# Optimization experiments

Hardware: AMD Instinct MI355X
Metric: run time of the kernel (lower is better)

## Reference

```python
import jax, jax.numpy as jnp
import numpy as np

EPS = 1e-5

def layer_norm(x, w):
    mu = x.mean(-1, keepdims=True)
    var = x.var(-1, keepdims=True)
    return (x - mu) * jax.lax.rsqrt(var + EPS) * w

def multihead_norm(x, w):
    # x: (B,S,NH,DH) -> group norm per head, elementwise weight over NH*DH features
    mu = x.mean(-1, keepdims=True)
    var = x.var(-1, keepdims=True)
    xn = (x - mu) * jax.lax.rsqrt(var + EPS)
    B, S, NH, DH = x.shape
    return xn.reshape(B, S, NH * DH) * w

def causal_conv1d(x, W, b):
    # x: (B,S,C), W: (C,K) depthwise causal conv, bias b: (C,)
    C, K = W.shape
    ker = W.T[:, None, :]  # (K,1,C) in WIO layout
    y = jax.lax.conv_general_dilated(x, ker, (1,), [(K - 1, 0)],
                                     dimension_numbers=('NWC', 'WIO', 'NWC'),
                                     feature_group_count=C)
    return y + b

def headwise_linear(x, W):
    # block-diagonal linear; W: (nblocks, out, in)
    nb, o, i = W.shape
    B, S, F = x.shape
    y = jnp.einsum('bsni,noi->bsno', x.reshape(B, S, nb, i), W)
    return y.reshape(B, S, nb * o)

def mlstm_block(x, ln_w, up_W, conv_W, conv_b, q_W, k_W, v_W, ig_W, ig_b, fg_W, fg_b, on_w, skip, down_W):
    B, S, E = x.shape
    I = up_W.shape[1] // 2
    NH = ig_W.shape[0]
    DH = I // NH
    xn = layer_norm(x, ln_w)
    up = xn @ up_W                       # (B,S,2I)
    xm, z = up[..., :I], up[..., I:]
    xc = jax.nn.silu(causal_conv1d(xm, conv_W, conv_b))
    q = headwise_linear(xc, q_W)
    k = headwise_linear(xc, k_W)
    v = headwise_linear(xm, v_W)        # values come from the pre-conv branch
    gin = jnp.concatenate([q, k, v], -1)  # (B,S,3I)
    ig = (gin @ ig_W.T + ig_b).transpose(0, 2, 1)  # (B,NH,S)
    fg = (gin @ fg_W.T + fg_b).transpose(0, 2, 1)
    qh = q.reshape(B, S, NH, DH).transpose(0, 2, 1, 3)
    kh = k.reshape(B, S, NH, DH).transpose(0, 2, 1, 3)
    vh = v.reshape(B, S, NH, DH).transpose(0, 2, 1, 3)
    # parallel stabilized mLSTM (matrix memory)
    logf = jax.nn.log_sigmoid(fg)
    cs = jnp.concatenate([jnp.zeros_like(logf[..., :1]), jnp.cumsum(logf, -1)], -1)  # (B,NH,S+1)
    lf = cs[..., 1:, None] - cs[..., None, 1:]   # (B,NH,S,S): sum of log f over (t, s]
    mask = jnp.tril(jnp.ones((S, S), bool))
    log_D = jnp.where(mask, lf + ig[:, :, None, :], -jnp.inf)
    max_log_D = log_D.max(-1, keepdims=True)
    D = jnp.exp(log_D - max_log_D)
    qk = jnp.einsum('bhsd,bhtd->bhst', qh, kh) * (DH ** -0.5)
    C = qk * D
    normalizer = jnp.maximum(jnp.abs(C.sum(-1, keepdims=True)), jnp.exp(-max_log_D))
    h = jnp.einsum('bhst,bhtd->bhsd', C / (normalizer + 1e-6), vh)
    h = multihead_norm(h.transpose(0, 2, 1, 3), on_w)  # (B,S,I)
    h = (h + skip * xc) * jax.nn.silu(z)
    return x + h @ down_W

def slstm_block(x, ln_w, conv_W, conv_b, gates_W, R, bias, gn_w, ffn_ln_w, ffn_up_W, ffn_down_W):
    B, S, E = x.shape
    NH, DH = R.shape[0], R.shape[1]
    xn = layer_norm(x, ln_w)
    xc = jax.nn.silu(causal_conv1d(xn, conv_W, conv_b))
    xh = xn.reshape(B, S, NH, DH)
    xch = xc.reshape(B, S, NH, DH)
    i_pre = jnp.einsum('bsnd,nod->bsno', xch, gates_W[0])  # i,f gates see conv branch
    f_pre = jnp.einsum('bsnd,nod->bsno', xch, gates_W[1])
    z_pre = jnp.einsum('bsnd,nod->bsno', xh, gates_W[2])
    o_pre = jnp.einsum('bsnd,nod->bsno', xh, gates_W[3])
    gx = jnp.stack([i_pre, f_pre, z_pre, o_pre], 3) + bias  # (B,S,NH,4,DH)
    def step(carry, g):
        h, c, n, m = carry
        raw = g + jnp.einsum('bnd,ndg->bng', h, R).reshape(B, NH, 4, DH)
        ir, fr, zr, og = raw[:, :, 0], raw[:, :, 1], raw[:, :, 2], raw[:, :, 3]
        logfplusm = m + jax.nn.log_sigmoid(fr)
        m_new = jnp.maximum(ir, logfplusm)
        i = jnp.exp(ir - m_new)
        f = jnp.exp(logfplusm - m_new)
        c_new = f * c + i * jnp.tanh(zr)
        n_new = f * n + i
        h_new = jax.nn.sigmoid(og) * c_new / n_new
        return (h_new, c_new, n_new, m_new), h_new
    z0 = jnp.zeros((B, NH, DH), x.dtype)
    _, hs = jax.lax.scan(step, (z0, z0, z0, z0), gx.transpose(1, 0, 2, 3, 4))
    y = multihead_norm(hs.transpose(1, 0, 2, 3), gn_w)  # (B,S,E)
    x = x + y
    xn2 = layer_norm(x, ffn_ln_w)
    gpre, upp = jnp.split(xn2 @ ffn_up_W, 2, -1)
    return x + (jax.nn.gelu(gpre, approximate=False) * upp) @ ffn_down_W

def forward(x, m_ln_w, m_up_W, m_conv_W, m_conv_b, m_q_W, m_k_W, m_v_W, m_ig_W, m_ig_b, m_fg_W, m_fg_b, m_outnorm_w, m_skip, m_down_W, s_ln_w, s_conv_W, s_conv_b, s_gates_W, s_R, s_bias, s_gn_w, s_ffn_ln_w, s_ffn_up_W, s_ffn_down_W, post_norm_w, fc_W, fc_b):
    mi = 0
    for blk in range(7):  # slstm_at=[1]
        if blk == 1:
            x = slstm_block(x, s_ln_w, s_conv_W, s_conv_b, s_gates_W, s_R, s_bias, s_gn_w, s_ffn_ln_w, s_ffn_up_W, s_ffn_down_W)
        else:
            x = mlstm_block(x, m_ln_w[mi], m_up_W[mi], m_conv_W[mi], m_conv_b[mi], m_q_W[mi], m_k_W[mi], m_v_W[mi], m_ig_W[mi], m_ig_b[mi], m_fg_W[mi], m_fg_b[mi], m_outnorm_w[mi], m_skip[mi], m_down_W[mi])
            mi += 1
    x = layer_norm(x, post_norm_w)
    return x[:, -1, :] @ fc_W + fc_b

def setup_inputs():
    key = jax.random.key(0)
    ks = jax.random.split(key, 18)
    B, S, E = 16, 512, 128
    I, NH = 256, 4
    DHs = E // NH
    FF = 192
    NB = 6
    r = lambda k, shape, sc: jax.random.normal(k, shape, jnp.float32) * sc
    return dict(
        x=r(ks[0], (B, S, E), 1.0),
        m_ln_w=jnp.ones((NB, E), jnp.float32),
        m_up_W=r(ks[1], (NB, E, 2 * I), E ** -0.5),
        m_conv_W=r(ks[2], (NB, I, 4), 0.3),
        m_conv_b=jnp.zeros((NB, I), jnp.float32),
        m_q_W=r(ks[3], (NB, 64, 4, 4), 0.5),
        m_k_W=r(ks[4], (NB, 64, 4, 4), 0.5),
        m_v_W=r(ks[5], (NB, 64, 4, 4), 0.5),
        m_ig_W=r(ks[6], (NB, NH, 3 * I), 0.1 * (3 * I) ** -0.5),
        m_ig_b=r(ks[7], (NB, NH), 0.5),
        m_fg_W=r(ks[8], (NB, NH, 3 * I), 0.1 * (3 * I) ** -0.5),
        m_fg_b=r(ks[9], (NB, NH), 1.0) + 3.0,
        m_outnorm_w=jnp.ones((NB, I), jnp.float32),
        m_skip=jnp.ones((NB, I), jnp.float32),
        m_down_W=r(ks[10], (NB, I, E), I ** -0.5),
        s_ln_w=jnp.ones((E,), jnp.float32),
        s_conv_W=r(ks[11], (E, 4), 0.3),
        s_conv_b=jnp.zeros((E,), jnp.float32),
        s_gates_W=r(ks[12], (4, NH, DHs, DHs), DHs ** -0.5),
        s_R=r(ks[13], (NH, DHs, 4 * DHs), 0.5 * DHs ** -0.5),
        s_bias=r(ks[14], (NH, 4, DHs), 0.1),
        s_gn_w=jnp.ones((E,), jnp.float32),
        s_ffn_ln_w=jnp.ones((E,), jnp.float32),
        s_ffn_up_W=r(ks[15], (E, 2 * FF), E ** -0.5),
        s_ffn_down_W=r(ks[16], (FF, E), FF ** -0.5),
        post_norm_w=jnp.ones((E,), jnp.float32),
        fc_W=r(ks[17], (E, 1), E ** -0.5),
        fc_b=jnp.zeros((1,), jnp.float32),
    )

def reference(x, m_ln_w, m_up_W, m_conv_W, m_conv_b, m_q_W, m_k_W, m_v_W, m_ig_W, m_ig_b, m_fg_W, m_fg_b, m_outnorm_w, m_skip, m_down_W, s_ln_w, s_conv_W, s_conv_b, s_gates_W, s_R, s_bias, s_gn_w, s_ffn_ln_w, s_ffn_up_W, s_ffn_down_W, post_norm_w, fc_W, fc_b):
    return forward(x, m_ln_w, m_up_W, m_conv_W, m_conv_b, m_q_W, m_k_W, m_v_W, m_ig_W, m_ig_b, m_fg_W, m_fg_b, m_outnorm_w, m_skip, m_down_W, s_ln_w, s_conv_W, s_conv_b, s_gates_W, s_R, s_bias, s_gn_w, s_ffn_ln_w, s_ffn_up_W, s_ffn_down_W, post_norm_w, fc_W, fc_b)
```

## Files before the change

kernel.cpp:

```cpp
#include <hip/hip_runtime.h>
#include <cstddef>

constexpr int B = 16, S = 512, E = 128, I = 256, DHm = 64;
constexpr int BS = B * S;

typedef _Float16 half8 __attribute__((ext_vector_type(8)));
typedef _Float16 half4 __attribute__((ext_vector_type(4)));
typedef float f32x4 __attribute__((ext_vector_type(4)));

__device__ __forceinline__ int swz(int row, int col) {
  return (row * 64 + col) ^ ((row & 7) << 3);
}
struct h3s { _Float16 a, b, c; };
__device__ __forceinline__ h3s split3(float x) {
  h3s r;
  r.a = (_Float16)x;
  float t = x - (float)r.a;
  r.b = (_Float16)t;
  t -= (float)r.b;
  r.c = (_Float16)t;
  return r;
}
struct h2s { _Float16 a, b; };
__device__ __forceinline__ h2s split2(float x) {
  h2s r;
  r.a = (_Float16)x;
  r.b = (_Float16)(x - (float)r.a);
  return r;
}

template <int K, bool ADD, int FUSE>
__global__ void __launch_bounds__(256) gemm3(const float* __restrict__ A,
                                             const float* __restrict__ W,
                                             const float* __restrict__ lnw,
                                             float* __restrict__ C, int N, int astride) {
  __shared__ _Float16 A1[4096], A2[4096];
  __shared__ _Float16 B1[4096], B2[4096];
  __shared__ float smu[64], srr[64];
  const int n0 = blockIdx.x * 64, m0 = blockIdx.y * 64;
  const int tid = threadIdx.x;
  const int lane = tid & 63, w = tid >> 6;
  const int sband = w * 16;
  const int fr = lane & 15, fg = lane >> 4;

  if constexpr (FUSE == 1) {
    int row = tid >> 2, q = tid & 3;
    const float* ap = A + (size_t)(m0 + row) * astride + q * 32;
    float s1 = 0.f, s2 = 0.f;
#pragma unroll
    for (int i = 0; i < 8; i++) {
      float4 v = *(const float4*)(ap + i * 4);
      s1 += v.x + v.y + v.z + v.w;
      s2 += v.x * v.x + v.y * v.y + v.z * v.z + v.w * v.w;
    }
    s1 += __shfl_xor(s1, 1); s2 += __shfl_xor(s2, 1);
    s1 += __shfl_xor(s1, 2); s2 += __shfl_xor(s2, 2);
    if (q == 0) {
      float mu = s1 * (1.f / 128);
      float var = s2 * (1.f / 128) - mu * mu;
      smu[row] = mu;
      srr[row] = rsqrtf(var + 1e-5f);
    }
  }

  f32x4 acc[4] = {};
#pragma unroll
  for (int k0 = 0; k0 < K; k0 += 64) {
    __syncthreads();
#pragma unroll
    for (int i = 0; i < 4; i++) {
      int lin = tid + i * 256;
      int mm = lin >> 4, kq = (lin & 15) * 4;
      float4 a4;
      if constexpr (FUSE == 2) {
        const float* ap = A + (size_t)(m0 + mm) * astride + k0 + kq;
        float4 g4 = *(const float4*)ap;
        float4 u4 = *(const float4*)(ap + 192);
        a4.x = 0.5f * g4.x * (1.f + erff(g4.x * 0.70710678118f)) * u4.x;
        a4.y = 0.5f * g4.y * (1.f + erff(g4.y * 0.70710678118f)) * u4.y;
        a4.z = 0.5f * g4.z * (1.f + erff(g4.z * 0.70710678118f)) * u4.z;
        a4.w = 0.5f * g4.w * (1.f + erff(g4.w * 0.70710678118f)) * u4.w;
      } else {
        a4 = *(const float4*)(A + (size_t)(m0 + mm) * astride + k0 + kq);
      }
      if constexpr (FUSE == 1) {
        float mu = smu[mm], rr = srr[mm];
        float4 wl = *(const float4*)(lnw + k0 + kq);
        a4.x = (a4.x - mu) * rr * wl.x;
        a4.y = (a4.y - mu) * rr * wl.y;
        a4.z = (a4.z - mu) * rr * wl.z;
        a4.w = (a4.w - mu) * rr * wl.w;
      }
      const float av[4] = {a4.x, a4.y, a4.z, a4.w};
      half4 h1, h2;
#pragma unroll
      for (int j = 0; j < 4; j++) {
        h2s sp = split2(av[j]);
        h1[j] = sp.a; h2[j] = sp.b;
      }
      *(half4*)&A1[swz(mm, kq)] = h1;
      *(half4*)&A2[swz(mm, kq)] = h2;
    }
#pragma unroll
    for (int i = 0; i < 4; i++) {
      int lin = tid + i * 256;
      int kk = lin >> 4, nq = (lin & 15) * 4;
      float4 w4 = *(const float4*)(W + (size_t)(k0 + kk) * N + n0 + nq);
      const float wv[4] = {w4.x, w4.y, w4.z, w4.w};
#pragma unroll
      for (int j = 0; j < 4; j++) {
        h2s sp = split2(wv[j]);
        B1[swz(nq + j, kk)] = sp.a;
        B2[swz(nq + j, kk)] = sp.b;
      }
    }
    __syncthreads();
    half8 a1g0 = *(const half8*)&A1[swz(sband + fr, fg * 8)];
    half8 a1g1 = *(const half8*)&A1[swz(sband + fr, 32 + fg * 8)];
    half8 a2g0 = *(const half8*)&A2[swz(sband + fr, fg * 8)];
    half8 a2g1 = *(const half8*)&A2[swz(sband + fr, 32 + fg * 8)];
#pragma unroll
    for (int ct = 0; ct < 4; ct++) {
      half8 b1g0 = *(const half8*)&B1[swz(ct * 16 + fr, fg * 8)];
      half8 b1g1 = *(const half8*)&B1[swz(ct * 16 + fr, 32 + fg * 8)];
      half8 b2g0 = *(const half8*)&B2[swz(ct * 16 + fr, fg * 8)];
      half8 b2g1 = *(const half8*)&B2[swz(ct * 16 + fr, 32 + fg * 8)];
      acc[ct] = __builtin_amdgcn_mfma_f32_16x16x32_f16(a2g0, b1g0, acc[ct], 0, 0, 0);
      acc[ct] = __builtin_amdgcn_mfma_f32_16x16x32_f16(a1g0, b2g0, acc[ct], 0, 0, 0);
      acc[ct] = __builtin_amdgcn_mfma_f32_16x16x32_f16(a1g0, b1g0, acc[ct], 0, 0, 0);
      acc[ct] = __builtin_amdgcn_mfma_f32_16x16x32_f16(a2g1, b1g1, acc[ct], 0, 0, 0);
      acc[ct] = __builtin_amdgcn_mfma_f32_16x16x32_f16(a1g1, b2g1, acc[ct], 0, 0, 0);
      acc[ct] = __builtin_amdgcn_mfma_f32_16x16x32_f16(a1g1, b1g1, acc[ct], 0, 0, 0);
    }
  }
#pragma unroll
  for (int ct = 0; ct < 4; ct++) {
#pragma unroll
    for (int r = 0; r < 4; r++) {
      int row = m0 + sband + fg * 4 + r;
      int col = n0 + ct * 16 + fr;
      float v = acc[ct][r];
      if (ADD) v += C[(size_t)row * N + col];
      C[(size_t)row * N + col] = v;
    }
  }
}

__global__ void __launch_bounds__(256) mlstm_mid_kernel(
    const float* __restrict__ UP, const float* __restrict__ conv_W,
    const float* __restrict__ conv_b, const float* __restrict__ qW,
    const float* __restrict__ kW, const float* __restrict__ vW,
    const float* __restrict__ igW, const float* __restrict__ igb,
    const float* __restrict__ fgW, const float* __restrict__ fgb,
    float* __restrict__ XC, float* __restrict__ Q, float* __restrict__ Kb,
    float* __restrict__ V, float* __restrict__ IG, float* __restrict__ FG) {
  __shared__ float xcl[I], xml[I], qkvl[768];
  __shared__ float red[32];
  int r = blockIdx.x, t = threadIdx.x;
  int s = r & (S - 1);
  const float* xr = UP + (size_t)r * 512 + t;
  float4 w4 = *(const float4*)(conv_W + t * 4);
  float x0 = xr[0];
  float acc = conv_b[t] + x0 * w4.w;
  if (s >= 1) acc += xr[-512] * w4.z;
  if (s >= 2) acc += xr[-1024] * w4.y;
  if (s >= 3) acc += xr[-1536] * w4.x;
  float xc = acc / (1.f + __expf(-acc));
  xcl[t] = xc;
  xml[t] = x0;
  XC[(size_t)r * I + t] = xc;
  __syncthreads();
  int n = t >> 2, o = t & 3;
  const float* qw = qW + n * 16 + o * 4;
  const float* kw = kW + n * 16 + o * 4;
  const float* vw = vW + n * 16 + o * 4;
  float q = 0, k = 0, v = 0;
#pragma unroll
  for (int i = 0; i < 4; i++) {
    float xcv = xcl[n * 4 + i], xmv = xml[n * 4 + i];
    q += xcv * qw[i]; k += xcv * kw[i]; v += xmv * vw[i];
  }
  Q[(size_t)r * I + t] = q;
  Kb[(size_t)r * I + t] = k;
  V[(size_t)r * I + t] = v;
  qkvl[t] = q; qkvl[256 + t] = k; qkvl[512 + t] = v;
  __syncthreads();
  float ai[4] = {}, af[4] = {};
#pragma unroll
  for (int j = 0; j < 3; j++) {
    int c = t + j * 256;
    float g = qkvl[c];
#pragma unroll
    for (int h = 0; h < 4; h++) {
      ai[h] += g * igW[h * 768 + c];
      af[h] += g * fgW[h * 768 + c];
    }
  }
#pragma unroll
  for (int m = 32; m; m >>= 1)
#pragma unroll
    for (int h = 0; h < 4; h++) {
      ai[h] += __shfl_xor(ai[h], m);
      af[h] += __shfl_xor(af[h], m);
    }
  int wv = t >> 6;
  if ((t & 63) == 0) {
#pragma unroll
    for (int h = 0; h < 4; h++) { red[wv * 8 + h] = ai[h]; red[wv * 8 + 4 + h] = af[h]; }
  }
  __syncthreads();
  if (t < 8) {
    float sum = red[t] + red[8 + t] + red[16 + t] + red[24 + t];
    int b = r >> 9, srow = r & (S - 1);
    int h = t & 3;
    if (t < 4) IG[((size_t)(b * 4 + h)) * S + srow] = sum + igb[h];
    else FG[((size_t)(b * 4 + h)) * S + srow] = sum + fgb[h];
  }
}

__global__ void __launch_bounds__(256) attn_mfma_kernel(
    const float* __restrict__ Q, const float* __restrict__ Kb, const float* __restrict__ V,
    const float* __restrict__ IG, const float* __restrict__ FG,
    const float* __restrict__ XC, const float* __restrict__ UP,
    const float* __restrict__ onw, const float* __restrict__ skip,
    float* __restrict__ HF) {
  __shared__ _Float16 K1[4096], K2[4096], K3[4096];
  __shared__ _Float16 V1[4096], V2[4096], V3[4096];
  __shared__ _Float16 W1[4096], W2[4096], W3[4096];
  __shared__ float A_l[512], M_l[512], F_l[512];
  int bid = blockIdx.x;
  int st = bid & 7, bh = bid >> 3;
  int b = bh >> 2, h = bh & 3;
  int s0 = st * 64;
  int tid = threadIdx.x;
  const float* Qg = Q + ((size_t)b * S) * I + h * DHm;
  const float* Kg = Kb + ((size_t)b * S) * I + h * DHm;
  const float* Vg = V + ((size_t)b * S) * I + h * DHm;

  const int lane = tid & 63, w = tid >> 6;
  const int sband = w * 16;
  const int fr = lane & 15, fg = lane >> 4;

  if (tid < 64) {
    int l = tid;
    const float* ig = IG + (size_t)bh * S;
    const float* fgp = FG + (size_t)bh * S;
    float lfc[8], av[8], amx[8];
    float cs = 0;
#pragma unroll
    for (int j = 0; j < 8; j++) {
      float f = fgp[l * 8 + j];
      cs += fminf(f, 0.f) - log1pf(__expf(-fabsf(f)));
      lfc[j] = cs;
    }
    float tot = cs, inc = tot;
#pragma unroll
    for (int off = 1; off < 64; off <<= 1) {
      float yv = __shfl_up(inc, off);
      if (l >= off) inc += yv;
    }
    float excl = inc - tot;
    float pm = -1e30f;
#pragma unroll
    for (int j = 0; j < 8; j++) {
      float CSj = excl + lfc[j];
      av[j] = ig[l * 8 + j] - CSj;
      pm = fmaxf(pm, av[j]);
      amx[j] = pm;
      lfc[j] = CSj;
    }
    float incm = pm;
#pragma unroll
    for (int off = 1; off < 64; off <<= 1) {
      float yv = __shfl_up(incm, off);
      if (l >= off) incm = fmaxf(incm, yv);
    }
    float exclm = __shfl_up(incm, 1);
    if (l == 0) exclm = -1e30f;
#pragma unroll
    for (int j = 0; j < 8; j++) {
      float Mj = fmaxf(exclm, amx[j]);
      A_l[l * 8 + j] = av[j];
      M_l[l * 8 + j] = Mj;
      F_l[l * 8 + j] = __expf(-(lfc[j] + Mj));
    }
  }

  half8 aq1[2], aq2[2], aq3[2];
  {
    const float* qrow = Qg + (size_t)(s0 + sband + fr) * I;
#pragma unroll
    for (int c = 0; c < 2; c++) {
      float4 qa = *(const float4*)(qrow + c * 32 + fg * 8);
      float4 qb = *(const float4*)(qrow + c * 32 + fg * 8 + 4);
      float qv[8] = {qa.x, qa.y, qa.z, qa.w, qb.x, qb.y, qb.z, qb.w};
#pragma unroll
      for (int j = 0; j < 8; j++) {
        h3s sp = split3(qv[j]);
        aq1[c][j] = sp.a; aq2[c][j] = sp.b; aq3[c][j] = sp.c;
      }
    }
  }
  __syncthreads();
  float msl[4];
#pragma unroll
  for (int r = 0; r < 4; r++) msl[r] = M_l[s0 + sband + fg * 4 + r];

  f32x4 hacc[4] = {};
  float csp[4] = {};

  for (int tt = 0; tt <= st; tt++) {
    int t0 = tt * 64;
    __syncthreads();
#pragma unroll
    for (int i = 0; i < 4; i++) {
      int lin = tid + i * 256;
      int t = lin >> 4, dq = (lin & 15) * 4;
      float4 kv = *(const float4*)(Kg + (size_t)(t0 + t) * I + dq);
      const float ka[4] = {kv.x, kv.y, kv.z, kv.w};
      half4 k1, k2, k3;
#pragma unroll
      for (int j = 0; j < 4; j++) {
        h3s sp = split3(ka[j]);
        k1[j] = sp.a; k2[j] = sp.b; k3[j] = sp.c;
      }
      *(half4*)&K1[swz(t, dq)] = k1;
      *(half4*)&K2[swz(t, dq)] = k2;
      *(half4*)&K3[swz(t, dq)] = k3;
      float4 vv = *(const float4*)(Vg + (size_t)(t0 + t) * I + dq);
      const float va[4] = {vv.x, vv.y, vv.z, vv.w};
#pragma unroll
      for (int j = 0; j < 4; j++) {
        h3s sp = split3(va[j]);
        V1[swz(dq + j, t)] = sp.a;
        V2[swz(dq + j, t)] = sp.b;
        V3[swz(dq + j, t)] = sp.c;
      }
    }
    __syncthreads();
#pragma unroll
    for (int ct = 0; ct < 4; ct++) {
      f32x4 sacc = {};
#pragma unroll
      for (int c = 0; c < 2; c++) {
        half8 b1 = *(const half8*)&K1[swz(ct * 16 + fr, c * 32 + fg * 8)];
        half8 b2 = *(const half8*)&K2[swz(ct * 16 + fr, c * 32 + fg * 8)];
        half8 b3 = *(const half8*)&K3[swz(ct * 16 + fr, c * 32 + fg * 8)];
        sacc = __builtin_amdgcn_mfma_f32_16x16x32_f16(aq3[c], b1, sacc, 0, 0, 0);
        sacc = __builtin_amdgcn_mfma_f32_16x16x32_f16(aq2[c], b2, sacc, 0, 0, 0);
        sacc = __builtin_amdgcn_mfma_f32_16x16x32_f16(aq1[c], b3, sacc, 0, 0, 0);
        sacc = __builtin_amdgcn_mfma_f32_16x16x32_f16(aq2[c], b1, sacc, 0, 0, 0);
        sacc = __builtin_amdgcn_mfma_f32_16x16x32_f16(aq1[c], b2, sacc, 0, 0, 0);
        sacc = __builtin_amdgcn_mfma_f32_16x16x32_f16(aq1[c], b1, sacc, 0, 0, 0);
      }
      int tg = t0 + ct * 16 + fr;
      float ea = A_l[tg];
#pragma unroll
      for (int r = 0; r < 4; r++) {
        int sl = sband + fg * 4 + r;
        float wv = 0.f;
        if (tg <= s0 + sl) wv = sacc[r] * 0.125f * __expf(ea - msl[r]);
        csp[r] += wv;
        h3s sp = split3(wv);
        W1[swz(sl, ct * 16 + fr)] = sp.a;
        W2[swz(sl, ct * 16 + fr)] = sp.b;
        W3[swz(sl, ct * 16 + fr)] = sp.c;
      }
    }
#pragma unroll
    for (int kc = 0; kc < 2; kc++) {
      half8 w1 = *(const half8*)&W1[swz(sband + fr, kc * 32 + fg * 8)];
      half8 w2 = *(const half8*)&W2[swz(sband + fr, kc * 32 + fg * 8)];
      half8 w3 = *(const half8*)&W3[swz(sband + fr, kc * 32 + fg * 8)];
#pragma unroll
      for (int dt = 0; dt < 4; dt++) {
        half8 v1 = *(const half8*)&V1[swz(dt * 16 + fr, kc * 32 + fg * 8)];
        half8 v2 = *(const half8*)&V2[swz(dt * 16 + fr, kc * 32 + fg * 8)];
        half8 v3 = *(const half8*)&V3[swz(dt * 16 + fr, kc * 32 + fg * 8)];
        hacc[dt] = __builtin_amdgcn_mfma_f32_16x16x32_f16(w3, v1, hacc[dt], 0, 0, 0);
        hacc[dt] = __builtin_amdgcn_mfma_f32_16x16x32_f16(w2, v2, hacc[dt], 0, 0, 0);
        hacc[dt] = __builtin_amdgcn_mfma_f32_16x16x32_f16(w1, v3, hacc[dt], 0, 0, 0);
        hacc[dt] = __builtin_amdgcn_mfma_f32_16x16x32_f16(w2, v1, hacc[dt], 0, 0, 0);
        hacc[dt] = __builtin_amdgcn_mfma_f32_16x16x32_f16(w1, v2, hacc[dt], 0, 0, 0);
        hacc[dt] = __builtin_amdgcn_mfma_f32_16x16x32_f16(w1, v1, hacc[dt], 0, 0, 0);
      }
    }
  }
#pragma unroll
  for (int m = 1; m < 16; m <<= 1)
#pragma unroll
    for (int r = 0; r < 4; r++) csp[r] += __shfl_xor(csp[r], m);
  float on4[4], sk4[4];
#pragma unroll
  for (int dt = 0; dt < 4; dt++) {
    on4[dt] = onw[h * DHm + dt * 16 + fr];
    sk4[dt] = skip[h * DHm + dt * 16 + fr];
  }
#pragma unroll
  for (int r = 0; r < 4; r++) {
    int sl = sband + fg * 4 + r;
    size_t row = (size_t)b * S + s0 + sl;
    float Fv = F_l[s0 + sl];
    float inv = 1.f / (fmaxf(fabsf(csp[r]), Fv) + 1e-6f);
    float hv[4], s1 = 0.f, s2 = 0.f;
#pragma unroll
    for (int dt = 0; dt < 4; dt++) {
      hv[dt] = hacc[dt][r] * inv;
      s1 += hv[dt];
      s2 += hv[dt] * hv[dt];
    }
#pragma unroll
    for (int m = 1; m < 16; m <<= 1) { s1 += __shfl_xor(s1, m); s2 += __shfl_xor(s2, m); }
    float mu = s1 * (1.f / 64), var = s2 * (1.f / 64) - mu * mu;
    float rr = rsqrtf(var + 1e-5f);
#pragma unroll
    for (int dt = 0; dt < 4; dt++) {
      int col = h * DHm + dt * 16 + fr;
      float xc = XC[row * I + col];
      float zv = UP[row * (2 * I) + I + col];
      float hn = (hv[dt] - mu) * rr * on4[dt];
      HF[row * I + col] = (hn + sk4[dt] * xc) * (zv / (1.f + __expf(-zv)));
    }
  }
}

__global__ void __launch_bounds__(512) slstm_pre_kernel(
    const float* __restrict__ X, const float* __restrict__ lnw,
    const float* __restrict__ conv_W, const float* __restrict__ conv_b,
    const float* __restrict__ gW, const float* __restrict__ bias,
    float* __restrict__ GX) {
  __shared__ float xnl[4][128], xcl[128];
  __shared__ float redS[8], redQ[8];
  int r = blockIdx.x, t = threadIdx.x;
  int s = r & (S - 1);
  int b0 = r - s;
  int rr = t >> 7, cc = t & 127;
  int sr = s - 3 + rr;
  int grow = b0 + (sr > 0 ? sr : 0);
  float x = X[(size_t)grow * E + cc];
  float s1 = x, s2 = x * x;
#pragma unroll
  for (int m = 32; m; m >>= 1) { s1 += __shfl_xor(s1, m); s2 += __shfl_xor(s2, m); }
  int wv = t >> 6;
  if ((t & 63) == 0) { redS[wv] = s1; redQ[wv] = s2; }
  __syncthreads();
  float fs1 = redS[rr * 2] + redS[rr * 2 + 1];
  float fs2 = redQ[rr * 2] + redQ[rr * 2 + 1];
  float mu = fs1 * (1.f / 128);
  float var = fs2 * (1.f / 128) - mu * mu;
  xnl[rr][cc] = (x - mu) * rsqrtf(var + 1e-5f) * lnw[cc];
  __syncthreads();
  if (t < 128) {
    float4 w4 = *(const float4*)(conv_W + t * 4);
    float acc = conv_b[t] + xnl[3][t] * w4.w;
    if (s >= 1) acc += xnl[2][t] * w4.z;
    if (s >= 2) acc += xnl[1][t] * w4.y;
    if (s >= 3) acc += xnl[0][t] * w4.x;
    xcl[t] = acc / (1.f + __expf(-acc));
  }
  __syncthreads();
  int n = t >> 7, g = (t >> 5) & 3, o = t & 31;
  const float* src = (g < 2) ? (xcl + n * 32) : (xnl[3] + n * 32);
  const float* wp = gW + (((size_t)g * 4 + n) * 32 + o) * 32;
  float acc = bias[n * 128 + g * 32 + o];
#pragma unroll
  for (int d = 0; d < 32; d++) acc += src[d] * wp[d];
  GX[(size_t)r * 512 + t] = acc;
}

__global__ void __launch_bounds__(128) slstm_scan8(const float* __restrict__ GX,
                                                   const float* __restrict__ R,
                                                   float* __restrict__ HS) {
  constexpr int CH = 16, NCH = S / CH;
  __shared__ float ring[2][CH][128];
  int blk = blockIdx.x;
  int b = blk >> 2, n = blk & 3;
  int tid = threadIdx.x;
  int wv = tid >> 6, l = tid & 63;
  const float* gxp = GX + ((size_t)b * S) * 512 + n * 128;

  float R0[32], R1[32];
  float h_own = 0.f, c = 0.f, nn = 0.f, m = 0.f;
  if (wv == 0) {
#pragma unroll
    for (int d = 0; d < 32; d++) {
      R0[d] = R[((size_t)(n * 32 + d)) * 128 + l];
      R1[d] = R[((size_t)(n * 32 + d)) * 128 + 64 + l];
    }
  } else {
    float v0[CH], v1[CH];
#pragma unroll
    for (int j = 0; j < CH; j++) {
      v0[j] = gxp[(size_t)j * 512 + l];
      v1[j] = gxp[(size_t)j * 512 + 64 + l];
    }
#pragma unroll
    for (int j = 0; j < CH; j++) {
      ring[0][j][l] = v0[j];
      ring[0][j][64 + l] = v1[j];
    }
  }
  __syncthreads();

  for (int ck = 0; ck < NCH; ck++) {
    if (wv == 1) {
      if (ck + 1 < NCH) {
        const float* src = gxp + (size_t)(ck + 1) * CH * 512;
        float v0[CH], v1[CH];
#pragma unroll
        for (int j = 0; j < CH; j++) {
          v0[j] = src[(size_t)j * 512 + l];
          v1[j] = src[(size_t)j * 512 + 64 + l];
        }
        int pb = (ck + 1) & 1;
#pragma unroll
        for (int j = 0; j < CH; j++) {
          ring[pb][j][l] = v0[j];
          ring[pb][j][64 + l] = v1[j];
        }
      }
    } else {
      int cb = ck & 1;
#pragma unroll
      for (int j = 0; j < CH; j++) {
        float g0 = ring[cb][j][l];
        float g1 = ring[cb][j][64 + l];
        float r0p0 = g0, r0p1 = 0.f, r0p2 = 0.f, r0p3 = 0.f;
        float r1p0 = g1, r1p1 = 0.f, r1p2 = 0.f, r1p3 = 0.f;
#pragma unroll
        for (int d = 0; d < 32; d += 4) {
          float hv0 = __shfl(h_own, d);
          float hv1 = __shfl(h_own, d + 1);
          float hv2 = __shfl(h_own, d + 2);
          float hv3 = __shfl(h_own, d + 3);
          r0p0 += hv0 * R0[d];     r1p0 += hv0 * R1[d];
          r0p1 += hv1 * R0[d + 1]; r1p1 += hv1 * R1[d + 1];
          r0p2 += hv2 * R0[d + 2]; r1p2 += hv2 * R1[d + 2];
          r0p3 += hv3 * R0[d + 3]; r1p3 += hv3 * R1[d + 3];
        }
        float raw0 = (r0p0 + r0p1) + (r0p2 + r0p3);
        float raw1 = (r1p0 + r1p1) + (r1p2 + r1p3);
        float fr = __shfl_down(raw0, 32);
        float og = __shfl_down(raw1, 32);
        float ir = raw0, zr = raw1;
        float lsf = fminf(fr, 0.f) - __logf(1.f + __expf(-fabsf(fr)));
        float lfm = m + lsf;
        float mn = fmaxf(ir, lfm);
        float iv = __expf(ir - mn), fv = __expf(lfm - mn);
        float th = 1.f - 2.f / (__expf(2.f * zr) + 1.f);
        c = fv * c + iv * th;
        nn = fv * nn + iv;
        m = mn;
        float hv = (c / nn) / (1.f + __expf(-og));
        h_own = hv;
        int s = ck * CH + j;
        if (l < 32) HS[((size_t)(b * S + s)) * E + n * 32 + l] = hv;
      }
    }
    __syncthreads();
  }
}

__global__ void gnorm_add_kernel(const float* __restrict__ HS, const float* __restrict__ gnw,
                                 float* __restrict__ X) {
  int r = blockIdx.x, t = threadIdx.x;
  float v = HS[(size_t)r * E + t];
  float s1 = v, s2 = v * v;
#pragma unroll
  for (int m = 16; m; m >>= 1) { s1 += __shfl_xor(s1, m, 32); s2 += __shfl_xor(s2, m, 32); }
  float mu = s1 * (1.f / 32), var = s2 * (1.f / 32) - mu * mu;
  X[(size_t)r * E + t] += (v - mu) * rsqrtf(var + 1e-5f) * gnw[t];
}

__global__ void head_kernel(const float* __restrict__ X, const float* __restrict__ pw,
                            const float* __restrict__ fcW, const float* __restrict__ fcb,
                            float* __restrict__ out) {
  int b = blockIdx.x, l = threadIdx.x;
  const float* xr = X + ((size_t)(b * S + S - 1)) * E;
  float2 v = *(const float2*)(xr + l * 2);
  float s1 = v.x + v.y, s2 = v.x * v.x + v.y * v.y;
#pragma unroll
  for (int m = 32; m; m >>= 1) { s1 += __shfl_xor(s1, m); s2 += __shfl_xor(s2, m); }
  float mu = s1 * (1.f / E), var = s2 * (1.f / E) - mu * mu;
  float rr = rsqrtf(var + 1e-5f);
  float2 wv = *(const float2*)(pw + l * 2);
  float2 fw = *(const float2*)(fcW + l * 2);
  float acc = (v.x - mu) * rr * wv.x * fw.x + (v.y - mu) * rr * wv.y * fw.y;
#pragma unroll
  for (int m = 32; m; m >>= 1) acc += __shfl_xor(acc, m);
  if (l == 0) out[b] = acc + fcb[0];
}

extern "C" void kernel_launch(void* const* d_in, const int* in_sizes, int n_in, void* d_out,
                              int out_size, void* d_ws, size_t ws_size, hipStream_t stream) {
  const float* in_x = (const float*)d_in[0];
  const float* m_ln_w = (const float*)d_in[1];
  const float* m_up_W = (const float*)d_in[2];
  const float* m_conv_W = (const float*)d_in[3];
  const float* m_conv_b = (const float*)d_in[4];
  const float* m_q_W = (const float*)d_in[5];
  const float* m_k_W = (const float*)d_in[6];
  const float* m_v_W = (const float*)d_in[7];
  const float* m_ig_W = (const float*)d_in[8];
  const float* m_ig_b = (const float*)d_in[9];
  const float* m_fg_W = (const float*)d_in[10];
  const float* m_fg_b = (const float*)d_in[11];
  const float* m_on_w = (const float*)d_in[12];
  const float* m_skip = (const float*)d_in[13];
  const float* m_down_W = (const float*)d_in[14];
  const float* s_ln_w = (const float*)d_in[15];
  const float* s_conv_W = (const float*)d_in[16];
  const float* s_conv_b = (const float*)d_in[17];
  const float* s_gates_W = (const float*)d_in[18];
  const float* s_R = (const float*)d_in[19];
  const float* s_bias = (const float*)d_in[20];
  const float* s_gn_w = (const float*)d_in[21];
  const float* s_ffn_ln_w = (const float*)d_in[22];
  const float* s_ffn_up_W = (const float*)d_in[23];
  const float* s_ffn_down_W = (const float*)d_in[24];
  const float* post_norm_w = (const float*)d_in[25];
  const float* fc_W = (const float*)d_in[26];
  const float* fc_b = (const float*)d_in[27];

  float* ws = (float*)d_ws;
  float* X = ws;
  float* XN = X + 1048576;
  float* UP = XN + 1048576;
  float* XC = UP + 4194304;
  float* Qb = XC + 2097152;
  float* Kb = Qb + 2097152;
  float* Vb = Kb + 2097152;
  float* Hb = Vb + 2097152;
  float* IGb = Hb + 2097152;
  float* FGb = IGb + 32768;

  hipMemcpyAsync(X, in_x, (size_t)BS * E * sizeof(float), hipMemcpyDeviceToDevice, stream);

  int mi = 0;
  for (int blk = 0; blk < 7; blk++) {
    if (blk == 1) {
      slstm_pre_kernel<<<BS, 512, 0, stream>>>(X, s_ln_w, s_conv_W, s_conv_b, s_gates_W,
                                               s_bias, UP);
      slstm_scan8<<<64, 128, 0, stream>>>(UP, s_R, Hb);
      gnorm_add_kernel<<<BS, E, 0, stream>>>(Hb, s_gn_w, X);
      gemm3<128, false, 1><<<dim3(6, 128), 256, 0, stream>>>(X, s_ffn_up_W, s_ffn_ln_w, UP,
                                                             384, 128);
      gemm3<192, true, 2><<<dim3(2, 128), 256, 0, stream>>>(UP, s_ffn_down_W, nullptr, X,
                                                            128, 384);
    } else {
      const float* ln_w = m_ln_w + (size_t)mi * E;
      const float* up_W = m_up_W + (size_t)mi * E * 512;
      const float* conv_W = m_conv_W + (size_t)mi * I * 4;
      const float* conv_b = m_conv_b + (size_t)mi * I;
      const float* q_W = m_q_W + (size_t)mi * 1024;
      const float* k_W = m_k_W + (size_t)mi * 1024;
      const float* v_W = m_v_W + (size_t)mi * 1024;
      const float* ig_W = m_ig_W + (size_t)mi * 3072;
      const float* ig_b = m_ig_b + (size_t)mi * 4;
      const float* fg_W = m_fg_W + (size_t)mi * 3072;
      const float* fg_b = m_fg_b + (size_t)mi * 4;
      const float* on_w = m_on_w + (size_t)mi * I;
      const float* skipv = m_skip + (size_t)mi * I;
      const float* down_W = m_down_W + (size_t)mi * I * E;

      gemm3<128, false, 1><<<dim3(8, 128), 256, 0, stream>>>(X, up_W, ln_w, UP, 512, 128);
      mlstm_mid_kernel<<<BS, 256, 0, stream>>>(UP, conv_W, conv_b, q_W, k_W, v_W, ig_W, ig_b,
                                               fg_W, fg_b, XC, Qb, Kb, Vb, IGb, FGb);
      attn_mfma_kernel<<<512, 256, 0, stream>>>(Qb, Kb, Vb, IGb, FGb, XC, UP, on_w, skipv,
                                                Hb);
      gemm3<256, true, 0><<<dim3(2, 128), 256, 0, stream>>>(Hb, down_W, nullptr, X, 128, 256);
      mi++;
    }
  }
  head_kernel<<<B, 64, 0, stream>>>(X, post_norm_w, fc_W, fc_b, (float*)d_out);
}
```

Baseline: 1.283 ms.

## Precompute fp16 three-way splits of K and transposed V in producer kernel

The mid kernel now splits K and V into three fp16 components once and writes them to global memory, with V stored transposed per head. The attention kernel then copies these halves straight into shared memory, so it no longer re-splits each K/V tile for every query tile that reads it. This trades repeated conversion work and fp32 reads for larger writes in the mid kernel (three halves per value) and scattered, uncoalesced transposed V stores.

```diff
diff --git a/kernel.cpp b/kernel.cpp
--- a/kernel.cpp
+++ b/kernel.cpp
@@ -152,8 +152,10 @@
     const float* __restrict__ kW, const float* __restrict__ vW,
     const float* __restrict__ igW, const float* __restrict__ igb,
     const float* __restrict__ fgW, const float* __restrict__ fgb,
-    float* __restrict__ XC, float* __restrict__ Q, float* __restrict__ Kb,
-    float* __restrict__ V, float* __restrict__ IG, float* __restrict__ FG) {
+    float* __restrict__ XC, float* __restrict__ Q,
+    _Float16* __restrict__ K1, _Float16* __restrict__ K2, _Float16* __restrict__ K3,
+    _Float16* __restrict__ V1t, _Float16* __restrict__ V2t, _Float16* __restrict__ V3t,
+    float* __restrict__ IG, float* __restrict__ FG) {
   __shared__ float xcl[I], xml[I], qkvl[768];
   __shared__ float red[32];
   int r = blockIdx.x, t = threadIdx.x;
@@ -181,8 +183,21 @@
     q += xcv * qw[i]; k += xcv * kw[i]; v += xmv * vw[i];
   }
   Q[(size_t)r * I + t] = q;
-  Kb[(size_t)r * I + t] = k;
-  V[(size_t)r * I + t] = v;
+  {
+    h3s sp = split3(k);
+    K1[(size_t)r * I + t] = sp.a;
+    K2[(size_t)r * I + t] = sp.b;
+    K3[(size_t)r * I + t] = sp.c;
+  }
+  {
+    int b = r >> 9, srow = r & (S - 1);
+    int h = t >> 6, d = t & 63;
+    size_t idx = ((size_t)(b * 4 + h) * 64 + d) * S + srow;
+    h3s sp = split3(v);
+    V1t[idx] = sp.a;
+    V2t[idx] = sp.b;
+    V3t[idx] = sp.c;
+  }
   qkvl[t] = q; qkvl[256 + t] = k; qkvl[512 + t] = v;
   __syncthreads();
   float ai[4] = {}, af[4] = {};
@@ -219,7 +234,10 @@
 }
 
 __global__ void __launch_bounds__(256) attn_mfma_kernel(
-    const float* __restrict__ Q, const float* __restrict__ Kb, const float* __restrict__ V,
+    const float* __restrict__ Q,
+    const _Float16* __restrict__ K1g, const _Float16* __restrict__ K2g,
+    const _Float16* __restrict__ K3g, const _Float16* __restrict__ V1g,
+    const _Float16* __restrict__ V2g, const _Float16* __restrict__ V3g,
     const float* __restrict__ IG, const float* __restrict__ FG,
     const float* __restrict__ XC, const float* __restrict__ UP,
     const float* __restrict__ onw, const float* __restrict__ skip,
@@ -234,8 +252,12 @@
   int s0 = st * 64;
   int tid = threadIdx.x;
   const float* Qg = Q + ((size_t)b * S) * I + h * DHm;
-  const float* Kg = Kb + ((size_t)b * S) * I + h * DHm;
-  const float* Vg = V + ((size_t)b * S) * I + h * DHm;
+  const _Float16* K1p = K1g + ((size_t)b * S) * I + h * DHm;
+  const _Float16* K2p = K2g + ((size_t)b * S) * I + h * DHm;
+  const _Float16* K3p = K3g + ((size_t)b * S) * I + h * DHm;
+  const _Float16* V1p = V1g + (size_t)bh * 64 * S;
+  const _Float16* V2p = V2g + (size_t)bh * 64 * S;
+  const _Float16* V3p = V3g + (size_t)bh * 64 * S;
 
   const int lane = tid & 63, w = tid >> 6;
   const int sband = w * 16;
@@ -315,27 +337,15 @@
 #pragma unroll
     for (int i = 0; i < 4; i++) {
       int lin = tid + i * 256;
-      int t = lin >> 4, dq = (lin & 15) * 4;
-      float4 kv = *(const float4*)(Kg + (size_t)(t0 + t) * I + dq);
-      const float ka[4] = {kv.x, kv.y, kv.z, kv.w};
-      half4 k1, k2, k3;
-#pragma unroll
-      for (int j = 0; j < 4; j++) {
-        h3s sp = split3(ka[j]);
-        k1[j] = sp.a; k2[j] = sp.b; k3[j] = sp.c;
-      }
-      *(half4*)&K1[swz(t, dq)] = k1;
-      *(half4*)&K2[swz(t, dq)] = k2;
-      *(half4*)&K3[swz(t, dq)] = k3;
-      float4 vv = *(const float4*)(Vg + (size_t)(t0 + t) * I + dq);
-      const float va[4] = {vv.x, vv.y, vv.z, vv.w};
-#pragma unroll
-      for (int j = 0; j < 4; j++) {
-        h3s sp = split3(va[j]);
-        V1[swz(dq + j, t)] = sp.a;
-        V2[swz(dq + j, t)] = sp.b;
-        V3[swz(dq + j, t)] = sp.c;
-      }
+      int a = lin >> 4, q4 = (lin & 15) * 4;
+      size_t koff = (size_t)(t0 + a) * I + q4;
+      *(half4*)&K1[swz(a, q4)] = *(const half4*)(K1p + koff);
+      *(half4*)&K2[swz(a, q4)] = *(const half4*)(K2p + koff);
+      *(half4*)&K3[swz(a, q4)] = *(const half4*)(K3p + koff);
+      size_t voff = (size_t)a * S + t0 + q4;
+      *(half4*)&V1[swz(a, q4)] = *(const half4*)(V1p + voff);
+      *(half4*)&V2[swz(a, q4)] = *(const half4*)(V2p + voff);
+      *(half4*)&V3[swz(a, q4)] = *(const half4*)(V3p + voff);
     }
     __syncthreads();
 #pragma unroll
@@ -624,15 +634,19 @@
 
   float* ws = (float*)d_ws;
   float* X = ws;
-  float* XN = X + 1048576;
-  float* UP = XN + 1048576;
+  float* UP = X + 1048576;
   float* XC = UP + 4194304;
   float* Qb = XC + 2097152;
-  float* Kb = Qb + 2097152;
-  float* Vb = Kb + 2097152;
-  float* Hb = Vb + 2097152;
+  float* Hb = Qb + 2097152;
   float* IGb = Hb + 2097152;
   float* FGb = IGb + 32768;
+  _Float16* F16 = (_Float16*)(FGb + 32768);
+  _Float16* K1 = F16;
+  _Float16* K2 = K1 + 2097152;
+  _Float16* K3 = K2 + 2097152;
+  _Float16* V1t = K3 + 2097152;
+  _Float16* V2t = V1t + 2097152;
+  _Float16* V3t = V2t + 2097152;
 
   hipMemcpyAsync(X, in_x, (size_t)BS * E * sizeof(float), hipMemcpyDeviceToDevice, stream);
 
@@ -665,9 +679,10 @@
 
       gemm3<128, false, 1><<<dim3(8, 128), 256, 0, stream>>>(X, up_W, ln_w, UP, 512, 128);
       mlstm_mid_kernel<<<BS, 256, 0, stream>>>(UP, conv_W, conv_b, q_W, k_W, v_W, ig_W, ig_b,
-                                               fg_W, fg_b, XC, Qb, Kb, Vb, IGb, FGb);
-      attn_mfma_kernel<<<512, 256, 0, stream>>>(Qb, Kb, Vb, IGb, FGb, XC, UP, on_w, skipv,
-                                                Hb);
+                                               fg_W, fg_b, XC, Qb, K1, K2, K3, V1t, V2t, V3t,
+                                               IGb, FGb);
+      attn_mfma_kernel<<<512, 256, 0, stream>>>(Qb, K1, K2, K3, V1t, V2t, V3t, IGb, FGb, XC,
+                                                UP, on_w, skipv, Hb);
       gemm3<256, true, 0><<<dim3(2, 128), 256, 0, stream>>>(Hb, down_W, nullptr, X, 128, 256);
       mi++;
     }
```

After: 1.279 ms. No clear change (-0.4%).
